# Performance work log

Hardware: AMD Instinct MI355X
Metric: run time of the kernel (lower is better)

The kernel has to match this reference:

```python
import jax, jax.numpy as jnp
import numpy as np

N_QUBITS = 14
DEPTH = 8
NUM_BLOCKS = DEPTH // 2
BATCH = 256
INIT_SCALE = 0.1


def _ry_mat(theta):
    # RY(t) = [[cos(t/2), -sin(t/2)], [sin(t/2), cos(t/2)]]; works for scalar or batched theta
    c = jnp.cos(theta / 2).astype(jnp.complex64)
    s = jnp.sin(theta / 2).astype(jnp.complex64)
    return jnp.stack([jnp.stack([c, -s], -1), jnp.stack([s, c], -1)], -2)


def _rz_mat(theta):
    # RZ(t) = diag(exp(-i t/2), exp(+i t/2))
    e = jnp.exp(-0.5j * theta.astype(jnp.complex64))
    z = jnp.zeros_like(e)
    return jnp.stack([jnp.stack([e, z], -1), jnp.stack([z, jnp.conj(e)], -1)], -2)


def _rx_mat(theta):
    # RX(t) = [[cos(t/2), -i sin(t/2)], [-i sin(t/2), cos(t/2)]] (target block of CRX)
    c = jnp.cos(theta / 2).astype(jnp.complex64)
    s = (-1j) * jnp.sin(theta / 2).astype(jnp.complex64)
    return jnp.stack([jnp.stack([c, s], -1), jnp.stack([s, c], -1)], -2)


def _apply_1q(state, mat, q, n):
    # state: (B, 2**n) complex64. Wire 0 = most significant axis (PennyLane convention).
    B = state.shape[0]
    s = state.reshape(B, 2 ** q, 2, 2 ** (n - q - 1))
    if mat.ndim == 3:  # per-sample angles (input encoding layer)
        out = jnp.einsum('bij,bljr->blir', mat, s)
    else:
        out = jnp.einsum('ij,bljr->blir', mat, s)
    return out.reshape(B, -1)


def _apply_ctrl(state, mat, c, t, n):
    # Apply 2x2 `mat` on target wire t where control wire c == 1.
    B = state.shape[0]
    s = state.reshape(B, 2 ** c, 2, 2 ** (n - c - 1))
    sub = s[:, :, 1, :]  # control = |1> subspace, (B, 2**c, 2**(n-c-1))
    p = t if t < c else t - 1  # target position in the reduced (n-1)-qubit register
    sub2 = sub.reshape(B, 2 ** p, 2, 2 ** (n - 2 - p))
    sub2 = jnp.einsum('ij,bljr->blir', mat, sub2)
    return s.at[:, :, 1, :].set(sub2.reshape(sub.shape)).reshape(B, -1)


def _circuit(inputs, weights):
    n, nb = N_QUBITS, NUM_BLOCKS
    B = inputs.shape[0]
    state = jnp.zeros((B, 2 ** n), jnp.complex64).at[:, 0].set(1.0)
    # input encoding: RY(inputs[..., q]) on each wire (batched angles)
    for q in range(n):
        state = _apply_1q(state, _ry_mat(inputs[:, q]), q, n)
    # weights flat index = b*3n + layer*n + q  ->  reshape (nb, 3, n)
    w = weights.reshape(nb, 3, n)
    X = jnp.asarray([[0, 1], [1, 0]], dtype=jnp.complex64)

    def block(st, wb):
        for q in range(n):
            st = _apply_1q(st, _ry_mat(wb[0, q]), q, n)
        for q in range(n):
            st = _apply_ctrl(st, X, q, (q + 1) % n, n)  # CNOT ring
        for q in range(n):
            st = _apply_1q(st, _rz_mat(wb[1, q]), q, n)
        for q in range(n):
            st = _apply_ctrl(st, _rx_mat(wb[2, q]), q, (q + 1) % n, n)  # CRX ring
        return st

    block = jax.checkpoint(block)
    for b in range(nb):
        state = block(state, w[b])

    # <Z_q> = P(bit_q = 0) - P(bit_q = 1)
    probs = state.real ** 2 + state.imag ** 2
    outs = []
    for q in range(n):
        pq = probs.reshape(B, 2 ** q, 2, -1)
        outs.append(pq[:, :, 0, :].sum((1, 2)) - pq[:, :, 1, :].sum((1, 2)))
    return jnp.stack(outs, -1).astype(jnp.float32)


def setup_inputs() -> dict:
    key = jax.random.key(0)
    k1, k2 = jax.random.split(key)
    inputs = jax.random.normal(k1, (BATCH, N_QUBITS), dtype=jnp.float32)
    weights = INIT_SCALE * jax.random.normal(k2, (3 * N_QUBITS * NUM_BLOCKS,), dtype=jnp.float32)
    return {"inputs": inputs, "weights": weights}


def reference(inputs, weights):
    return _circuit(inputs, weights)
```

## Files before the change

kernel.cpp:

```cpp
#include <hip/hip_runtime.h>
#include <utility>

#define NQ 14
#define NST (1 << NQ)
#define THREADS 1024
#define NP 16
#define NE 16

typedef float f2 __attribute__((ext_vector_type(2)));

struct PassD {
    unsigned short comboR[NE];
    unsigned short rows[5];
    unsigned short tmask[5];
    unsigned short crx_widx[4];
    unsigned short ry_widx[4];
    unsigned char  ry_tb[4];
    unsigned char  ncrx;
    unsigned char  nry;
    short          rzidx;
    unsigned char  measfold;
};
struct RZD  { unsigned short rows_ng[9]; unsigned short widx_ng[9]; unsigned short widx_g[5]; };
struct AllD { PassD pass[NP]; RZD rz[4]; unsigned short meas_rows_ng[9]; int npass; };

constexpr void fill_geom(PassD& P, const unsigned short* R, const unsigned short* C, const int* tb)
{
    for (int i = 0; i < 5; ++i) { P.tmask[i] = C[tb[i]]; P.rows[i] = R[tb[i]]; }
    for (int j = 0; j < NE; ++j) {
        unsigned short x = 0;
        for (int i = 0; i < 4; ++i) if ((j >> i) & 1) x = (unsigned short)(x ^ P.tmask[i]);
        P.comboR[j] = x;
    }
}

constexpr void ring(unsigned short* R, unsigned short* C) {
    for (int q = 0; q < NQ; ++q) {
        int cb = 13 - q, tb = 13 - ((q + 1) % NQ);
        R[tb] = (unsigned short)(R[tb] ^ R[cb]);
        C[cb] = (unsigned short)(C[cb] ^ C[tb]);
    }
}

constexpr AllD build_desc() {
    AllD A{};
    unsigned short R[NQ] = {}, C[NQ] = {};
    for (int k = 0; k < NQ; ++k) { R[k] = (unsigned short)(1u << k); C[k] = (unsigned short)(1u << k); }
    int np = 0;
    const int tiles[4][5]  = {{13,12,11,10,9},{9,8,7,6,5},{5,4,3,2,1},{1,0,13,3,2}};
    const int gfirst[4]    = {0, 4, 8, 12};
    const int ngate[4]     = {4, 4, 4, 2};
    const int rybits[4][4] = {{12,11,10,0},{9,8,7,6},{5,4,3,2},{13,1,0,0}};
    const int nryp[4]      = {3, 4, 4, 3};

    for (int blk = 0; blk < 4; ++blk) {
        ring(R, C);
        for (int pi = 0; pi < 4; ++pi) {
            PassD& P = A.pass[np];
            fill_geom(P, R, C, tiles[pi]);
            P.ncrx = (unsigned char)ngate[pi];
            for (int g = 0; g < 4; ++g)
                P.crx_widx[g] = (unsigned short)((g < ngate[pi]) ? blk*42 + 28 + gfirst[pi] + g : 0);
            if (blk < 3) {
                P.nry = (unsigned char)nryp[pi];
                for (int g = 0; g < 4; ++g) {
                    if (g < nryp[pi]) {
                        int k = rybits[pi][g];
                        P.ry_widx[g] = (unsigned short)((blk + 1)*42 + (13 - k));
                        int t = 0;
                        for (int i = 0; i < 5; ++i) if (tiles[pi][i] == k) t = i;
                        P.ry_tb[g] = (unsigned char)t;
                    } else { P.ry_widx[g] = 0; P.ry_tb[g] = 0; }
                }
            } else { P.nry = 0; for (int g = 0; g < 4; ++g) { P.ry_widx[g] = 0; P.ry_tb[g] = 0; } }
            P.rzidx = (short)((pi == 0) ? blk : -1);
            P.measfold = (unsigned char)((blk == 3 && pi == 3) ? 1 : 0);
            if (pi == 0) {
                RZD& Z = A.rz[blk];
                for (int i = 0; i < 5; ++i)
                    Z.widx_g[i] = (unsigned short)(blk*42 + 14 + (13 - tiles[0][i]));
                int t = 0;
                for (int q = 5; q < NQ; ++q, ++t) {
                    Z.rows_ng[t] = R[13 - q];
                    Z.widx_ng[t] = (unsigned short)(blk*42 + 14 + q);
                }
            }
            ++np;
        }
        if (blk == 3)
            for (int t = 0; t < 9; ++t) A.meas_rows_ng[t] = R[13 - (1 + t)];
    }
    A.npass = np;
    return A;
}

constexpr AllD A = build_desc();
static_assert(A.npass == NP, "expected 16 passes");

constexpr int parity14(unsigned v) { v ^= v >> 8; v ^= v >> 4; v ^= v >> 2; v ^= v >> 1; return (int)(v & 1); }

constexpr bool check_dual() {
    for (int p = 0; p < NP; ++p)
        for (int i = 0; i < 5; ++i)
            for (int j = 0; j < 5; ++j)
                if (parity14((unsigned)(A.pass[p].rows[i] & A.pass[p].tmask[j])) != (i == j ? 1 : 0))
                    return false;
    return true;
}
static_assert(check_dual(), "R/C duality violated");

constexpr bool check_ry() {
    for (int p = 0; p < NP; ++p)
        for (int g = 0; g < A.pass[p].nry; ++g)
            if (A.pass[p].ry_tb[g] > 3) return false;
    return true;
}
static_assert(check_ry(), "RY fold on lane bit not supported");

struct GWT { unsigned short w[NP][8]; };
constexpr GWT build_gwt() {
    GWT g{};
    for (int p = 0; p < NP; ++p) {
        for (int s = 0; s < 4; ++s) g.w[p][s]     = A.pass[p].crx_widx[s];
        for (int s = 0; s < 4; ++s) g.w[p][4 + s] = A.pass[p].ry_widx[s];
    }
    return g;
}
constexpr GWT GW = build_gwt();

constexpr int lead(unsigned short v) { int b = 13; while (b > 0 && !((v >> b) & 1)) --b; return b; }

struct Span {
    unsigned short red[14]; int n;
    constexpr unsigned short reduce(unsigned short v) const {
        for (int i = 0; i < n; ++i) { int lb = lead(red[i]); if ((v >> lb) & 1) v = (unsigned short)(v ^ red[i]); }
        return v;
    }
    constexpr bool add(unsigned short v) {
        unsigned short r = reduce(v);
        if (!r) return false;
        red[n++] = r; return true;
    }
};

constexpr unsigned short proj(unsigned short vec, const PassD& P) {
    unsigned short r = vec;
    for (int t = 0; t < 4; ++t)
        if (parity14((unsigned)(vec & P.rows[t]))) r = (unsigned short)(r ^ P.tmask[t]);
    return r;
}

struct VecsT { unsigned short lane[NP][6]; unsigned short g[NP/2][4]; int ok; };
constexpr VecsT build_vecs() {
    VecsT V{}; V.ok = 1;
    for (int k = 0; k < NP/2; ++k) {
        const PassD& P0 = A.pass[2*k];
        const PassD& P1 = A.pass[2*k + 1];
        Span SW{}; unsigned short Wb[10] = {}; int nw = 0;
        for (int i = 0; i < 5; ++i) if (SW.add(P0.tmask[i])) Wb[nw++] = P0.tmask[i];
        for (int i = 0; i < 5; ++i) if (nw < 10 && SW.add(P1.tmask[i])) Wb[nw++] = P1.tmask[i];
        for (int b = 0; b < 14 && nw < 10; ++b) {
            unsigned short e = (unsigned short)(1u << b);
            if (SW.add(e)) Wb[nw++] = e;
        }
        if (nw != 10) V.ok = 0;
        Span SG = SW; int ngv = 0;
        for (int b = 0; b < 14 && ngv < 4; ++b) {
            unsigned short e = (unsigned short)(1u << b);
            if (SG.add(e)) V.g[k][ngv++] = e;
        }
        if (ngv != 4) V.ok = 0;
        for (int pp = 0; pp < 2; ++pp) {
            const PassD& P = (pp == 0) ? P0 : P1;
            int pidx = 2*k + pp;
            Span ST{};
            for (int i = 0; i < 4; ++i) ST.add(P.tmask[i]);
            int nl = 0;
            if (ST.add(P.tmask[4])) V.lane[pidx][nl++] = P.tmask[4];
            else V.ok = 0;
            for (int i = 0; i < 10 && nl < 6; ++i)
                if (ST.add(Wb[i])) V.lane[pidx][nl++] = Wb[i];
            if (nl != 6) V.ok = 0;
            Span SF{};
            for (int i = 0; i < 4; ++i) SF.add(P.tmask[i]);
            for (int i = 0; i < 6; ++i) if (!SF.add(V.lane[pidx][i])) V.ok = 0;
            for (int i = 0; i < 4; ++i) if (!SF.add(V.g[k][i])) V.ok = 0;
            if (SF.n != 14) V.ok = 0;
        }
    }
    return V;
}
constexpr VecsT VC = build_vecs();
static_assert(VC.ok == 1, "vec construction failed");

struct P6T { unsigned short u[NP][6]; };
constexpr P6T build_p6() {
    P6T X{};
    for (int p = 0; p < NP; ++p)
        for (int i = 0; i < 6; ++i)
            X.u[p][i] = proj(VC.lane[p][i], A.pass[p]);
    return X;
}
constexpr P6T P6 = build_p6();

constexpr unsigned lmap(const unsigned short* row, unsigned x) {
    unsigned l = 0;
    for (int t = 0; t < 4; ++t) l |= (unsigned)parity14(row[t] & x) << t;
    return l;
}
constexpr int nib_rank(const unsigned* nibs, int n) {
    unsigned basis[4] = {};
    int r = 0;
    for (int i = 0; i < n; ++i) {
        unsigned v = nibs[i] & 15u;
        for (int b = 3; b >= 0 && v; --b) {
            if (!((v >> b) & 1)) continue;
            if (basis[b]) v ^= basis[b];
            else { basis[b] = v; ++r; v = 0; }
        }
    }
    return r;
}
struct Lp { unsigned short row[4]; int score; };

constexpr int full_score(const unsigned short* r) {
    unsigned cn[4] = {};
    for (int c = 0; c < 4; ++c) {
        unsigned v = 0;
        for (int t = 0; t < 4; ++t) v |= ((unsigned)(r[t] >> c) & 1u) << t;
        cn[c] = v;
    }
    if (nib_rank(cn, 4) != 4) return -1;
    int sc = 0;
    for (int p = 0; p < NP; ++p) {
        unsigned im[6] = {};
        for (int i = 0; i < 6; ++i) im[i] = lmap(r, P6.u[p][i]);
        if (nib_rank(im, 6) == 4) ++sc;
    }
    return sc;
}

constexpr Lp search_stage(unsigned seed, int iters) {
    Lp best{}; best.score = -1;
    unsigned s = seed;
    for (int it = 0; it < iters; ++it) {
        unsigned short r[4] = {};
        for (int t = 0; t < 4; ++t) { s = s*1664525u + 1013904223u; r[t] = (unsigned short)((s >> 9) & 0x3FFF); }
        int sc = full_score(r);
        if (sc > best.score) { best.score = sc; for (int t = 0; t < 4; ++t) best.row[t] = r[t]; }
        if (best.score == NP) break;
    }
    return best;
}
constexpr Lp S0 = search_stage(0x12345u, 400);
constexpr Lp S1 = search_stage(0xBEEF1u, 400);
constexpr Lp S2 = search_stage(0xC0FFEu, 400);
constexpr Lp S3 = search_stage(0x777A1u, 400);
constexpr Lp S4 = search_stage(0x51DE5u, 400);
constexpr Lp S5 = search_stage(0xA11CEu, 400);
constexpr Lp S6 = search_stage(0x0F00Du, 400);
constexpr Lp S7 = search_stage(0x13579u, 400);
constexpr Lp pick_best() {
    Lp b = S0;
    if (S1.score > b.score) b = S1;
    if (S2.score > b.score) b = S2;
    if (S3.score > b.score) b = S3;
    if (S4.score > b.score) b = S4;
    if (S5.score > b.score) b = S5;
    if (S6.score > b.score) b = S6;
    if (S7.score > b.score) b = S7;
    return b;
}
constexpr Lp climb(Lp start, int sweeps) {
    Lp cur = start;
    for (int sw = 0; sw < sweeps && cur.score < NP; ++sw) {
        for (int t = 0; t < 4; ++t) {
            for (int b = 0; b < 14; ++b) {
                if (cur.score >= NP) break;
                unsigned short nr[4] = {cur.row[0], cur.row[1], cur.row[2], cur.row[3]};
                nr[t] = (unsigned short)(nr[t] ^ (1u << b));
                int sc = full_score(nr);
                if (sc > cur.score) { cur.score = sc; cur.row[t] = nr[t]; }
            }
        }
    }
    return cur;
}
constexpr Lp C0 = climb(pick_best(), 2);
constexpr Lp C1 = climb(C0, 2);
constexpr Lp LSEL = C1;
static_assert(LSEL.score >= 13, "bank-map search failed badly");

constexpr unsigned short swz2(unsigned short x) {
    return (unsigned short)(((unsigned)x & ~15u) | lmap(LSEL.row, x));
}

constexpr int add_basis4(unsigned* basis, unsigned v) {
    for (int b = 3; b >= 0; --b) {
        if (!((v >> b) & 1)) continue;
        if (basis[b]) v ^= basis[b];
        else { basis[b] = v; return 1; }
    }
    return 0;
}
constexpr int add_basis6(unsigned* basis, unsigned v) {
    for (int b = 5; b >= 0; --b) {
        if (!((v >> b) & 1)) continue;
        if (basis[b]) v ^= basis[b];
        else { basis[b] = v; return 1; }
    }
    return 0;
}
struct LaneOrd { unsigned short lane[NP][6]; };
constexpr LaneOrd build_lane2() {
    LaneOrd O{};
    for (int p = 0; p < NP; ++p) {
        for (int i = 0; i < 6; ++i) O.lane[p][i] = VC.lane[p][i];
        unsigned imu[6] = {};
        for (int i = 0; i < 6; ++i) imu[i] = lmap(LSEL.row, P6.u[p][i]);
        {
            unsigned chk[6] = {imu[0], imu[1], imu[2], imu[3], imu[4], imu[5]};
            if (nib_rank(chk, 6) != 4) continue;
        }
        unsigned short nl[6] = {};
        int ns = 0;
        unsigned ib[4] = {};
        unsigned sb[6] = {};
        for (unsigned c = 1; c < 64 && ns < 4; ++c) {
            unsigned img = 0; unsigned short rv = 0;
            for (int i = 0; i < 6; ++i) if ((c >> i) & 1) { img ^= imu[i]; rv = (unsigned short)(rv ^ VC.lane[p][i]); }
            if (img == 0) continue;
            unsigned ib2[4] = {ib[0], ib[1], ib[2], ib[3]};
            unsigned sb2[6] = {sb[0], sb[1], sb[2], sb[3], sb[4], sb[5]};
            if (add_basis4(ib2, img) && add_basis6(sb2, c)) {
                for (int t = 0; t < 4; ++t) ib[t] = ib2[t];
                for (int t = 0; t < 6; ++t) sb[t] = sb2[t];
                nl[ns++] = rv;
            }
        }
        for (unsigned c = 1; c < 64 && ns < 6; ++c) {
            unsigned img = 0; unsigned short rv = 0;
            for (int i = 0; i < 6; ++i) if ((c >> i) & 1) { img ^= imu[i]; rv = (unsigned short)(rv ^ VC.lane[p][i]); }
            if (img != 0) continue;
            unsigned sb2[6] = {sb[0], sb[1], sb[2], sb[3], sb[4], sb[5]};
            if (add_basis6(sb2, c)) {
                for (int t = 0; t < 6; ++t) sb[t] = sb2[t];
                nl[ns++] = rv;
            }
        }
        if (ns == 6)
            for (int i = 0; i < 6; ++i) O.lane[p][i] = nl[i];
    }
    return O;
}
constexpr LaneOrd LO = build_lane2();

struct SHMt { int m[NP]; int ok; };
constexpr SHMt build_shm() {
    SHMt S{}; S.ok = 1;
    for (int p = 0; p < NP; ++p) {
        S.m[p] = 0;
        if (A.pass[p].ncrx < 4) continue;
        int found = 0;
        for (unsigned c = 1; c < 64 && !found; ++c) {
            unsigned short x = 0;
            for (int i = 0; i < 6; ++i) if ((c >> i) & 1) x = (unsigned short)(x ^ LO.lane[p][i]);
            if (x == A.pass[p].tmask[4]) { S.m[p] = (int)c; found = 1; }
        }
        if (!found) S.ok = 0;
    }
    return S;
}
constexpr SHMt SHM = build_shm();
static_assert(SHM.ok == 1, "shuffle mask not found");

struct CS2 { unsigned short c[NP][NE]; };
constexpr CS2 build_cs2() {
    CS2 C{};
    for (int p = 0; p < NP; ++p)
        for (int j = 0; j < NE; ++j)
            C.c[p][j] = swz2(A.pass[p].comboR[j]);
    return C;
}
constexpr CS2 CSS = build_cs2();

struct LJt { unsigned short v[NE]; };
constexpr LJt build_lj() {
    LJt t{};
    for (int j = 0; j < NE; ++j) t.v[j] = (unsigned short)lmap(LSEL.row, (unsigned)(j * THREADS));
    return t;
}
constexpr LJt LJ = build_lj();

constexpr unsigned pack_entry(unsigned short vec0, int p) {
    const PassD& P = A.pass[p];
    unsigned short vec = proj(vec0, P);
    unsigned par = 0;
    if (P.rzidx >= 0)
        for (int t = 0; t < 9; ++t) par |= (unsigned)parity14(vec & A.rz[P.rzidx].rows_ng[t]) << t;
    if (P.measfold)
        for (int t = 0; t < 9; ++t) par |= (unsigned)parity14(vec & A.meas_rows_ng[t]) << t;
    par |= (unsigned)parity14(vec & P.rows[4]) << 9;
    return ((unsigned)swz2(vec) << 3) | (par << 22);
}

struct LutsT { unsigned v[NP][2][32]; };
constexpr LutsT build_luts() {
    LutsT L{};
    for (int p = 0; p < NP; ++p) {
        int k = p >> 1;
        for (int t = 0; t < 32; ++t) {
            unsigned short x = 0;
            for (int i = 0; i < 5; ++i) if ((t >> i) & 1) x = (unsigned short)(x ^ LO.lane[p][i]);
            L.v[p][0][t] = pack_entry(x, p);
            unsigned short y = 0;
            if (t & 1) y = (unsigned short)(y ^ LO.lane[p][5]);
            for (int i = 0; i < 4; ++i) if ((t >> (i + 1)) & 1) y = (unsigned short)(y ^ VC.g[k][i]);
            L.v[p][1][t] = pack_entry(y, p);
        }
    }
    return L;
}
constexpr LutsT LUTS = build_luts();
__device__ __constant__ LutsT cLUTS = LUTS;

template<int Pi>
__device__ __forceinline__ void run_pass(f2* st, const f2 (*tabG)[8], const float (*tabRZ)[14],
                                         unsigned comb, float* acc)
{
    constexpr PassD Pd = A.pass[Pi];
    char* stb = (char*)st;
    const int base = (int)(comb & 0x1FFF8u);
    const unsigned par = comb >> 22;

    f2 v[NE];
#pragma unroll
    for (int j = 0; j < NE; ++j)
        v[j] = *(const f2*)(stb + (base ^ (CSS.c[Pi][j] << 3)));

    if constexpr (Pd.rzidx >= 0) {
        float phi0 = 0.f;
#pragma unroll
        for (int t = 0; t < 9; ++t) {
            float h = tabRZ[Pd.rzidx][t];
            phi0 += ((par >> t) & 1) ? h : -h;
        }
        { float h = tabRZ[Pd.rzidx][13]; phi0 += ((par >> 9) & 1) ? h : -h; }
        const float h0 = tabRZ[Pd.rzidx][9],  h1 = tabRZ[Pd.rzidx][10];
        const float h2 = tabRZ[Pd.rzidx][11], h3 = tabRZ[Pd.rzidx][12];
#pragma unroll
        for (int j = 0; j < NE; ++j) {
            float phi = ((((phi0 + ((j & 1) ? h0 : -h0)) + ((j & 2) ? h1 : -h1))
                                 + ((j & 4) ? h2 : -h2)) + ((j & 8) ? h3 : -h3));
            float s, c; __sincosf(phi, &s, &c);
            f2 C = {c, c}, S = {-s, s};
            v[j] = C * v[j] + S * v[j].yx;
        }
    }

#pragma unroll
    for (int g = 0; g < (Pd.ncrx < 3 ? (int)Pd.ncrx : 3); ++g) {
        f2 cs = tabG[Pi][g];
        f2 C = {cs.x, cs.x}, S = {cs.y, -cs.y};
#pragma unroll
        for (int j = 0; j < NE; ++j) if (((j >> g) & 1) && !((j >> (g + 1)) & 1)) {
            int j1 = j | (1 << (g + 1));
            f2 a0 = v[j], a1 = v[j1];
            v[j]  = C * a0 + S * a1.yx;
            v[j1] = C * a1 + S * a0.yx;
        }
    }
    if constexpr (Pd.ncrx == 4) {
        constexpr int sm = SHM.m[Pi];
        f2 cs = tabG[Pi][3];
        f2 C = {cs.x, cs.x}, S = {cs.y, -cs.y};
#pragma unroll
        for (int j = 8; j < 16; ++j) {
            f2 pv;
            pv.x = __shfl_xor(v[j].x, sm, 64);
            pv.y = __shfl_xor(v[j].y, sm, 64);
            v[j] = C * v[j] + S * pv.yx;
        }
    }

#pragma unroll
    for (int g = 0; g < Pd.nry; ++g) {
        int t = Pd.ry_tb[g];
        f2 cs = tabG[Pi][4 + g];
        f2 C = {cs.x, cs.x}, Sv = {cs.y, cs.y}, NS = {-cs.y, -cs.y};
#pragma unroll
        for (int j = 0; j < NE; ++j) if (!((j >> t) & 1)) {
            int j1 = j | (1 << t);
            f2 a0 = v[j], a1 = v[j1];
            v[j]  = C * a0 + NS * a1;
            v[j1] = Sv * a0 + C * a1;
        }
    }

    if constexpr (Pd.measfold != 0) {
        f2 ps = {0.f, 0.f}, p0 = {0.f, 0.f}, p1 = {0.f, 0.f}, p2 = {0.f, 0.f}, p3 = {0.f, 0.f};
#pragma unroll
        for (int j = 0; j < NE; ++j) {
            f2 t2 = v[j] * v[j];
            ps += t2;
            if (j & 1) p0 += t2;
            if (j & 2) p1 += t2;
            if (j & 4) p2 += t2;
            if (j & 8) p3 += t2;
        }
        float psum = ps.x + ps.y;
        float pg0 = p0.x + p0.y, pg1 = p1.x + p1.y, pg2 = p2.x + p2.y, pg3 = p3.x + p3.y;
        acc[12] += psum - 2.f * pg0;
        acc[13] += psum - 2.f * pg1;
        acc[0]  += psum - 2.f * pg2;
        acc[10] += psum - 2.f * pg3;
        float s4 = ((par >> 9) & 1) ? -1.f : 1.f;
        acc[11] += s4 * psum;
#pragma unroll
        for (int t = 0; t < 9; ++t) {
            float sg = ((par >> t) & 1) ? -1.f : 1.f;
            acc[1 + t] += sg * psum;
        }
    } else {
#pragma unroll
        for (int j = 0; j < NE; ++j)
            *(f2*)(stb + (base ^ (CSS.c[Pi][j] << 3))) = v[j];
        if constexpr ((Pi & 1) != 0) __syncthreads();
    }
}

template<int... I>
__device__ __forceinline__ void run_all(std::integer_sequence<int, I...>,
                                        f2* st, const f2 (*tabG)[8], const float (*tabRZ)[14],
                                        const unsigned* comb, float* acc)
{
    (run_pass<I>(st, tabG, tabRZ, comb[I], acc), ...);
}

__global__ __launch_bounds__(THREADS, 4)
void qsim_kernel(const float* __restrict__ inputs,
                 const float* __restrict__ weights,
                 float* __restrict__ out)
{
    __shared__ f2     st[NST];
    __shared__ float  tab[256];
    __shared__ f2     tabG[NP][8];
    __shared__ float  tabRZ[4][14];
    __shared__ float  red[THREADS / 64][NQ];

    const int b = blockIdx.x;
    const int tid = threadIdx.x;

    unsigned comb[NP];
#pragma unroll
    for (int p = 0; p < NP; ++p)
        comb[p] = cLUTS.v[p][0][tid & 31] ^ cLUTS.v[p][1][tid >> 5];

    if (tid < 128) {
        int p = tid >> 3, sl = tid & 7;
        float w = weights[GW.w[p][sl]];
        float s, c; __sincosf(0.5f * w, &s, &c);
        tabG[p][sl] = (f2){c, s};
    } else if (tid >= 128 && tid < 128 + 56) {
        int idx = tid - 128;
        int blk = idx / 14, k = idx - blk * 14;
        unsigned wi = (k < 9) ? A.rz[blk].widx_ng[k] : A.rz[blk].widx_g[k - 9];
        tabRZ[blk][k] = 0.5f * weights[wi];
    } else if (tid >= 256 && tid < 512) {
        int t = tid - 256;
        int half = t >> 7, tt = t & 127;
        float prod = 1.f;
#pragma unroll
        for (int j = 0; j < 7; ++j) {
            int xb = j + 7 * half;
            int q  = 13 - xb;
            float a = 0.5f * (inputs[b * NQ + q] + weights[q]);
            float s, c; __sincosf(a, &s, &c);
            prod *= ((tt >> j) & 1) ? s : c;
        }
        tab[t] = prod;
    }
    __syncthreads();

    unsigned l4t = 0;
#pragma unroll
    for (int t = 0; t < 4; ++t)
        l4t |= (unsigned)(__popc((int)(LSEL.row[t] & tid)) & 1) << t;
#pragma unroll
    for (int j = 0; j < NE; ++j) {
        int x = tid + j * THREADS;
        int addr = (x & ~15) | (int)(l4t ^ LJ.v[j]);
        st[addr] = (f2){tab[x & 127] * tab[128 + (x >> 7)], 0.f};
    }
    __syncthreads();

    float acc[NQ];
#pragma unroll
    for (int q = 0; q < NQ; ++q) acc[q] = 0.f;

    run_all(std::make_integer_sequence<int, NP>{}, st, tabG, tabRZ, comb, acc);

#pragma unroll
    for (int q = 0; q < NQ; ++q) {
        float v2 = acc[q];
        v2 += __shfl_down(v2, 32);
        v2 += __shfl_down(v2, 16);
        v2 += __shfl_down(v2, 8);
        v2 += __shfl_down(v2, 4);
        v2 += __shfl_down(v2, 2);
        v2 += __shfl_down(v2, 1);
        acc[q] = v2;
    }
    const int wave = tid >> 6, lane = tid & 63;
    if (lane == 0) {
#pragma unroll
        for (int q = 0; q < NQ; ++q) red[wave][q] = acc[q];
    }
    __syncthreads();
    if (tid < NQ) {
        float v2 = 0.f;
#pragma unroll
        for (int w = 0; w < THREADS / 64; ++w) v2 += red[w][tid];
        out[b * NQ + tid] = v2;
    }
}

extern "C" void kernel_launch(void* const* d_in, const int* in_sizes, int n_in,
                              void* d_out, int out_size, void* d_ws, size_t ws_size,
                              hipStream_t stream) {
    const float* inputs  = (const float*)d_in[0];
    const float* weights = (const float*)d_in[1];
    float* out = (float*)d_out;
    const int B = in_sizes[0] / NQ;
    qsim_kernel<<<dim3(B), dim3(THREADS), 0, stream>>>(inputs, weights, out);
}
```

Baseline: 47.88 us.

## Remap pass tiles so one qubit per pass is lane-resident and gates fold

Reassigns the five-qubit tiles per pass so that the first tile bit lives across lanes rather than in registers, changing the register combo masks, RZ/measurement index maps and the last pass's tile. CRX gates controlled on the lane bit become per-lane conditional rotations, and the shuffle-based gate moves from a CRX on 8 elements to an RY across all 16 elements, folding an extra RY into the last pass. This rebalances the gate schedule across passes to cut total work or shuffles, at the cost of more shuffles in the last pass and a more intricate index mapping.

```diff
diff --git a/kernel.cpp b/kernel.cpp
--- a/kernel.cpp
+++ b/kernel.cpp
@@ -15,8 +15,11 @@
     unsigned short tmask[5];
     unsigned short crx_widx[4];
     unsigned short ry_widx[4];
+    unsigned short shry_widx;
     unsigned char  ry_tb[4];
-    unsigned char  ncrx;
+    unsigned char  ngl;
+    unsigned char  has_g0;
+    unsigned char  has_shry;
     unsigned char  nry;
     short          rzidx;
     unsigned char  measfold;
@@ -29,7 +32,7 @@
     for (int i = 0; i < 5; ++i) { P.tmask[i] = C[tb[i]]; P.rows[i] = R[tb[i]]; }
     for (int j = 0; j < NE; ++j) {
         unsigned short x = 0;
-        for (int i = 0; i < 4; ++i) if ((j >> i) & 1) x = (unsigned short)(x ^ P.tmask[i]);
+        for (int i = 1; i < 5; ++i) if ((j >> (i - 1)) & 1) x = (unsigned short)(x ^ P.tmask[i]);
         P.comboR[j] = x;
     }
 }
@@ -47,38 +50,49 @@
     unsigned short R[NQ] = {}, C[NQ] = {};
     for (int k = 0; k < NQ; ++k) { R[k] = (unsigned short)(1u << k); C[k] = (unsigned short)(1u << k); }
     int np = 0;
-    const int tiles[4][5]  = {{13,12,11,10,9},{9,8,7,6,5},{5,4,3,2,1},{1,0,13,3,2}};
-    const int gfirst[4]    = {0, 4, 8, 12};
-    const int ngate[4]     = {4, 4, 4, 2};
-    const int rybits[4][4] = {{12,11,10,0},{9,8,7,6},{5,4,3,2},{13,1,0,0}};
-    const int nryp[4]      = {3, 4, 4, 3};
+    const int tiles[4][5]  = {{13,12,11,10,9},{9,8,7,6,5},{5,4,3,2,1},{9,1,0,13,5}};
+    const int fb[4][4] = {{12,11,10,0},{8,7,6,0},{4,3,2,0},{1,0,13,5}};
+    const int nf[4]    = {3,3,3,4};
 
     for (int blk = 0; blk < 4; ++blk) {
         ring(R, C);
         for (int pi = 0; pi < 4; ++pi) {
             PassD& P = A.pass[np];
             fill_geom(P, R, C, tiles[pi]);
-            P.ncrx = (unsigned char)ngate[pi];
-            for (int g = 0; g < 4; ++g)
-                P.crx_widx[g] = (unsigned short)((g < ngate[pi]) ? blk*42 + 28 + gfirst[pi] + g : 0);
+            if (pi < 3) {
+                P.has_g0 = 1; P.ngl = 3;
+                for (int g = 0; g < 4; ++g) P.crx_widx[g] = (unsigned short)(blk*42 + 28 + 4*pi + g);
+            } else {
+                P.has_g0 = 0; P.ngl = 2;
+                P.crx_widx[0] = 0;
+                P.crx_widx[1] = (unsigned short)(blk*42 + 28 + 12);
+                P.crx_widx[2] = (unsigned short)(blk*42 + 28 + 13);
+                P.crx_widx[3] = 0;
+            }
             if (blk < 3) {
-                P.nry = (unsigned char)nryp[pi];
+                P.nry = (unsigned char)nf[pi];
                 for (int g = 0; g < 4; ++g) {
-                    if (g < nryp[pi]) {
-                        int k = rybits[pi][g];
+                    if (g < nf[pi]) {
+                        int k = fb[pi][g];
                         P.ry_widx[g] = (unsigned short)((blk + 1)*42 + (13 - k));
                         int t = 0;
-                        for (int i = 0; i < 5; ++i) if (tiles[pi][i] == k) t = i;
+                        for (int i = 1; i < 5; ++i) if (tiles[pi][i] == k) t = i - 1;
                         P.ry_tb[g] = (unsigned char)t;
                     } else { P.ry_widx[g] = 0; P.ry_tb[g] = 0; }
                 }
-            } else { P.nry = 0; for (int g = 0; g < 4; ++g) { P.ry_widx[g] = 0; P.ry_tb[g] = 0; } }
+                P.has_shry = (unsigned char)((pi == 3) ? 1 : 0);
+                P.shry_widx = (unsigned short)((blk + 1)*42 + 4);
+            } else {
+                P.nry = 0; P.has_shry = 0; P.shry_widx = 0;
+                for (int g = 0; g < 4; ++g) { P.ry_widx[g] = 0; P.ry_tb[g] = 0; }
+            }
             P.rzidx = (short)((pi == 0) ? blk : -1);
             P.measfold = (unsigned char)((blk == 3 && pi == 3) ? 1 : 0);
             if (pi == 0) {
                 RZD& Z = A.rz[blk];
-                for (int i = 0; i < 5; ++i)
-                    Z.widx_g[i] = (unsigned short)(blk*42 + 14 + (13 - tiles[0][i]));
+                for (int i = 0; i < 4; ++i)
+                    Z.widx_g[i] = (unsigned short)(blk*42 + 14 + (13 - tiles[0][i + 1]));
+                Z.widx_g[4] = (unsigned short)(blk*42 + 14 + 0);
                 int t = 0;
                 for (int q = 5; q < NQ; ++q, ++t) {
                     Z.rows_ng[t] = R[13 - q];
@@ -87,8 +101,10 @@
             }
             ++np;
         }
-        if (blk == 3)
-            for (int t = 0; t < 9; ++t) A.meas_rows_ng[t] = R[13 - (1 + t)];
+        if (blk == 3) {
+            const int MQ[9] = {1,2,3,5,6,7,9,10,11};
+            for (int t = 0; t < 9; ++t) A.meas_rows_ng[t] = R[13 - MQ[t]];
+        }
     }
     A.npass = np;
     return A;
@@ -115,13 +131,16 @@
             if (A.pass[p].ry_tb[g] > 3) return false;
     return true;
 }
-static_assert(check_ry(), "RY fold on lane bit not supported");
+static_assert(check_ry(), "RY fold must be on local position");
 
 struct GWT { unsigned short w[NP][8]; };
 constexpr GWT build_gwt() {
     GWT g{};
     for (int p = 0; p < NP; ++p) {
-        for (int s = 0; s < 4; ++s) g.w[p][s]     = A.pass[p].crx_widx[s];
+        g.w[p][0] = A.pass[p].crx_widx[0];
+        g.w[p][1] = A.pass[p].crx_widx[1];
+        g.w[p][2] = A.pass[p].crx_widx[2];
+        g.w[p][3] = A.pass[p].has_shry ? A.pass[p].shry_widx : A.pass[p].crx_widx[3];
         for (int s = 0; s < 4; ++s) g.w[p][4 + s] = A.pass[p].ry_widx[s];
     }
     return g;
@@ -145,7 +164,7 @@
 
 constexpr unsigned short proj(unsigned short vec, const PassD& P) {
     unsigned short r = vec;
-    for (int t = 0; t < 4; ++t)
+    for (int t = 1; t < 5; ++t)
         if (parity14((unsigned)(vec & P.rows[t]))) r = (unsigned short)(r ^ P.tmask[t]);
     return r;
 }
@@ -174,15 +193,15 @@
             const PassD& P = (pp == 0) ? P0 : P1;
             int pidx = 2*k + pp;
             Span ST{};
-            for (int i = 0; i < 4; ++i) ST.add(P.tmask[i]);
+            for (int i = 1; i < 5; ++i) ST.add(P.tmask[i]);
             int nl = 0;
-            if (ST.add(P.tmask[4])) V.lane[pidx][nl++] = P.tmask[4];
+            if (ST.add(P.tmask[0])) V.lane[pidx][nl++] = P.tmask[0];
             else V.ok = 0;
             for (int i = 0; i < 10 && nl < 6; ++i)
                 if (ST.add(Wb[i])) V.lane[pidx][nl++] = Wb[i];
             if (nl != 6) V.ok = 0;
             Span SF{};
-            for (int i = 0; i < 4; ++i) SF.add(P.tmask[i]);
+            for (int i = 1; i < 5; ++i) SF.add(P.tmask[i]);
             for (int i = 0; i < 6; ++i) if (!SF.add(V.lane[pidx][i])) V.ok = 0;
             for (int i = 0; i < 4; ++i) if (!SF.add(V.g[k][i])) V.ok = 0;
             if (SF.n != 14) V.ok = 0;
@@ -360,12 +379,12 @@
     SHMt S{}; S.ok = 1;
     for (int p = 0; p < NP; ++p) {
         S.m[p] = 0;
-        if (A.pass[p].ncrx < 4) continue;
+        if (!A.pass[p].has_shry) continue;
         int found = 0;
         for (unsigned c = 1; c < 64 && !found; ++c) {
             unsigned short x = 0;
             for (int i = 0; i < 6; ++i) if ((c >> i) & 1) x = (unsigned short)(x ^ LO.lane[p][i]);
-            if (x == A.pass[p].tmask[4]) { S.m[p] = (int)c; found = 1; }
+            if (x == A.pass[p].tmask[0]) { S.m[p] = (int)c; found = 1; }
         }
         if (!found) S.ok = 0;
     }
@@ -400,7 +419,7 @@
         for (int t = 0; t < 9; ++t) par |= (unsigned)parity14(vec & A.rz[P.rzidx].rows_ng[t]) << t;
     if (P.measfold)
         for (int t = 0; t < 9; ++t) par |= (unsigned)parity14(vec & A.meas_rows_ng[t]) << t;
-    par |= (unsigned)parity14(vec & P.rows[4]) << 9;
+    par |= (unsigned)parity14(vec & P.rows[0]) << 9;
     return ((unsigned)swz2(vec) << 3) | (par << 22);
 }
 
@@ -458,28 +477,30 @@
         }
     }
 
-#pragma unroll
-    for (int g = 0; g < (Pd.ncrx < 3 ? (int)Pd.ncrx : 3); ++g) {
-        f2 cs = tabG[Pi][g];
-        f2 C = {cs.x, cs.x}, S = {cs.y, -cs.y};
-#pragma unroll
-        for (int j = 0; j < NE; ++j) if (((j >> g) & 1) && !((j >> (g + 1)) & 1)) {
-            int j1 = j | (1 << (g + 1));
+    if constexpr (Pd.has_g0) {
+        f2 cs = tabG[Pi][0];
+        int s4v = (int)((par >> 9) & 1);
+        float ce = s4v ? cs.x : 1.f, se = s4v ? cs.y : 0.f;
+        f2 C = {ce, ce}, S = {se, -se};
+#pragma unroll
+        for (int j = 0; j < NE; ++j) if (!(j & 1)) {
+            int j1 = j | 1;
             f2 a0 = v[j], a1 = v[j1];
             v[j]  = C * a0 + S * a1.yx;
             v[j1] = C * a1 + S * a0.yx;
         }
     }
-    if constexpr (Pd.ncrx == 4) {
-        constexpr int sm = SHM.m[Pi];
-        f2 cs = tabG[Pi][3];
+
+#pragma unroll
+    for (int lg = 0; lg < Pd.ngl; ++lg) {
+        f2 cs = tabG[Pi][1 + lg];
         f2 C = {cs.x, cs.x}, S = {cs.y, -cs.y};
 #pragma unroll
-        for (int j = 8; j < 16; ++j) {
-            f2 pv;
-            pv.x = __shfl_xor(v[j].x, sm, 64);
-            pv.y = __shfl_xor(v[j].y, sm, 64);
-            v[j] = C * v[j] + S * pv.yx;
+        for (int j = 0; j < NE; ++j) if (((j >> lg) & 1) && !((j >> (lg + 1)) & 1)) {
+            int j1 = j | (1 << (lg + 1));
+            f2 a0 = v[j], a1 = v[j1];
+            v[j]  = C * a0 + S * a1.yx;
+            v[j1] = C * a1 + S * a0.yx;
         }
     }
 
@@ -494,6 +515,21 @@
             f2 a0 = v[j], a1 = v[j1];
             v[j]  = C * a0 + NS * a1;
             v[j1] = Sv * a0 + C * a1;
+        }
+    }
+
+    if constexpr (Pd.has_shry) {
+        constexpr int sm = SHM.m[Pi];
+        f2 cs = tabG[Pi][3];
+        int s4v = (int)((par >> 9) & 1);
+        float se = s4v ? cs.y : -cs.y;
+        f2 C = {cs.x, cs.x}, S = {se, se};
+#pragma unroll
+        for (int j = 0; j < NE; ++j) {
+            f2 pv;
+            pv.x = __shfl_xor(v[j].x, sm, 64);
+            pv.y = __shfl_xor(v[j].y, sm, 64);
+            v[j] = C * v[j] + S * pv;
         }
     }
 
@@ -513,13 +549,14 @@
         acc[12] += psum - 2.f * pg0;
         acc[13] += psum - 2.f * pg1;
         acc[0]  += psum - 2.f * pg2;
-        acc[10] += psum - 2.f * pg3;
+        acc[8]  += psum - 2.f * pg3;
         float s4 = ((par >> 9) & 1) ? -1.f : 1.f;
-        acc[11] += s4 * psum;
+        acc[4] += s4 * psum;
+        constexpr int MQ[9] = {1,2,3,5,6,7,9,10,11};
 #pragma unroll
         for (int t = 0; t < 9; ++t) {
             float sg = ((par >> t) & 1) ? -1.f : 1.f;
-            acc[1 + t] += sg * psum;
+            acc[MQ[t]] += sg * psum;
         }
     } else {
 #pragma unroll
```

Result: faster. 44.63 us (-6.8%).
